# Kernel tuning notes

Measured on AMD Instinct MI355X. Metric: run time of the kernel, lower is better.

## Reference

```python
import jax, jax.numpy as jnp
import numpy as np

NEG = -1e6  # matches torch masked value of -1000000.0
EPS = 1e-5


def setup_inputs() -> dict:
    key = jax.random.key(0)
    k1, k2, k3, k4, k5, k6 = jax.random.split(key, 6)
    B, H, L, D = 2, 16, 2048, 128
    BH = B * H
    return {
        "queries": jax.random.normal(k1, (BH, L, D), dtype=jnp.float32),
        "keys": jax.random.normal(k2, (BH, L, D), dtype=jnp.float32),
        "values": jax.random.normal(k3, (BH, L, D), dtype=jnp.float32),
        "q_mult": jax.random.normal(k4, (B, L, D), dtype=jnp.float32),
        "kv_mult": jax.random.normal(k5, (B, L, D), dtype=jnp.float32),
        "valid_lens": jax.random.randint(k6, (BH,), 0, L, dtype=jnp.int64),
        "num_heads": 16,
    }


def reference(queries, keys, values, q_mult, kv_mult, valid_lens, num_heads):
    # queries/keys/values: [BH, L, d]; q_mult/kv_mult: [B, L, d_m]; valid_lens: [BH]
    d = queries.shape[-1]
    Lk = keys.shape[1]
    scale = 1.0 / jnp.sqrt(jnp.asarray(d, dtype=queries.dtype))
    scores = jnp.einsum('bqd,bkd->bqk', queries, keys) * scale  # [BH, Lq, Lk]

    # custom additive multiplicative-interaction term, Frobenius-normalized per batch element
    mult_ = jnp.einsum('bqd,bkd->bqk', q_mult, kv_mult)  # [B, Lq, Lk]
    fro = jnp.sqrt(jnp.sum(mult_ * mult_, axis=(1, 2), keepdims=True))
    mult_ = mult_ / (fro + EPS)
    mult_ = jnp.repeat(mult_, num_heads, axis=0)  # [BH, Lq, Lk]

    # masked softmax over keys: valid_lens is per-(batch*head), broadcast over queries
    key_mask = jnp.arange(Lk)[None, None, :] < valid_lens[:, None, None]  # [BH, 1, Lk]
    scores = jnp.where(key_mask, scores, NEG)
    attn = jax.nn.softmax(scores, axis=-1) + mult_  # after_softmax=True path

    # dropout is identity (p=0 / eval)
    return jnp.einsum('bqk,bkd->bqd', attn, values)
```

## Files before the change

kernel.cpp:

```cpp
#include <hip/hip_runtime.h>


typedef __attribute__((ext_vector_type(8))) __bf16 bf16x8;
typedef __attribute__((ext_vector_type(16))) float f32x16;
typedef __attribute__((ext_vector_type(4))) unsigned int u32x4;

#define DEV static __device__ __forceinline__

constexpr int LL = 2048, DD = 128, BH = 32;
constexpr float SCALE = 0.08838834764831845f;
constexpr float NEGV = -1e6f;

DEV unsigned pkb(float a, float b) {
  union { __bf16 h[2]; unsigned u; } x;
  x.h[0] = (__bf16)a; x.h[1] = (__bf16)b;
  return x.u;
}
DEV f32x16 mfma32(bf16x8 a, bf16x8 b, f32x16 c) {
  return __builtin_amdgcn_mfma_f32_32x32x16_bf16(a, b, c, 0, 0, 0);
}
DEV void gl16(const void* g, void* l) {
  __builtin_amdgcn_global_load_lds(
      (const __attribute__((address_space(1))) unsigned int*)g,
      (__attribute__((address_space(3))) unsigned int*)l, 16, 0, 0);
}

__global__ __launch_bounds__(256)
void mega_pre(const float* __restrict__ K, const float* __restrict__ V,
              const float* __restrict__ qm, const float* __restrict__ km,
              char* __restrict__ Kb, char* __restrict__ Vt,
              float* __restrict__ Gq, float* __restrict__ Gk,
              float* __restrict__ Mp) {
  __shared__ __align__(16) char smem[16384];
  const int bx = blockIdx.x, tid = threadIdx.x;

  if (bx < 512) {
    float (*skv)[64] = (float(*)[64])smem;
    float (*sv)[128] = (float(*)[128])(smem + 4096);
    int bh = bx & 31, b = bh >> 4, kc = (bx >> 5) & 7, z = (bx >> 8) & 1;
    int l0 = kc * 256;
    int j0 = (tid & 31) * 4, i0 = (tid >> 5) * 8;
    float acc[8][4];
#pragma unroll
    for (int i = 0; i < 8; ++i)
#pragma unroll
      for (int qq = 0; qq < 4; ++qq) acc[i][qq] = 0.f;
    for (int c = 0; c < 16; ++c) {
      __syncthreads();
      {
        int rr = tid >> 4, c4 = (tid & 15) * 4;
        *(float4*)&skv[rr][c4] =
            *(const float4*)(km + (size_t)(b * LL + l0 + c * 16 + rr) * DD + z * 64 + c4);
#pragma unroll
        for (int x = 0; x < 2; ++x) {
          int id2 = x * 256 + tid;
          int r2 = id2 >> 5, c42 = (id2 & 31) * 4;
          *(float4*)&sv[r2][c42] =
              *(const float4*)(V + (size_t)(bh * LL + l0 + c * 16 + r2) * DD + c42);
        }
      }
      __syncthreads();
#pragma unroll
      for (int ll = 0; ll < 16; ++ll) {
        float4 a = *(const float4*)&sv[ll][j0];
        float4 k0 = *(const float4*)&skv[ll][i0];
        float4 k1 = *(const float4*)&skv[ll][i0 + 4];
        float kk[8] = {k0.x, k0.y, k0.z, k0.w, k1.x, k1.y, k1.z, k1.w};
#pragma unroll
        for (int ii = 0; ii < 8; ++ii) {
          acc[ii][0] += kk[ii] * a.x;
          acc[ii][1] += kk[ii] * a.y;
          acc[ii][2] += kk[ii] * a.z;
          acc[ii][3] += kk[ii] * a.w;
        }
      }
    }
    float* dst = Mp + (((size_t)bh * 8 + kc) << 14) + (size_t)(z * 64 + i0) * 128 + j0;
#pragma unroll
    for (int ii = 0; ii < 8; ++ii)
      *(float4*)(dst + (size_t)ii * 128) = *(float4*)&acc[ii][0];

  } else if (bx < 640) {
    float (*s)[128] = (float(*)[128])smem;
    int g = bx - 512;
    int ib = g & 7, lc = (g >> 3) & 3, wb = g >> 5;
    int which = wb >> 1, b = wb & 1;
    const float* A = (which ? km : qm) + (size_t)b * LL * DD;
    float* G = (which ? Gk : Gq) + (size_t)b * DD * DD;
    int i0 = ib * 16 + (tid >> 7) * 8, j = tid & 127;
    int l0 = lc * 512;
    float acc[8];
#pragma unroll
    for (int i = 0; i < 8; ++i) acc[i] = 0.f;
    for (int ch = 0; ch < 16; ++ch) {
      __syncthreads();
#pragma unroll
      for (int i = 0; i < 4; ++i) {
        int c = i * 256 + tid;
        int row = c >> 5, c4 = (c & 31) * 4;
        *(float4*)&s[row][c4] =
            *(const float4*)(A + (size_t)(l0 + ch * 32 + row) * DD + c4);
      }
      __syncthreads();
#pragma unroll
      for (int ll = 0; ll < 32; ++ll) {
        float aj = s[ll][j];
#pragma unroll
        for (int ii = 0; ii < 8; ++ii) acc[ii] += s[ll][i0 + ii] * aj;
      }
    }
#pragma unroll
    for (int ii = 0; ii < 8; ++ii)
      atomicAdd(&G[(size_t)(i0 + ii) * DD + j], acc[ii]);

  } else if (bx < 1664) {
    int pk = bx - 640;
#pragma unroll
    for (int i = 0; i < 4; ++i) {
      int cid = i * 262144 + pk * 256 + tid;
      int h = cid >> 15, k = (cid >> 4) & 2047, c = cid & 15;
      const float* p = K + ((size_t)h * LL + k) * DD + c * 8;
      float4 x0 = *(const float4*)p, x1 = *(const float4*)(p + 4);
      u32x4 v;
      v.x = pkb(x0.x, x0.y); v.y = pkb(x0.z, x0.w);
      v.z = pkb(x1.x, x1.y); v.w = pkb(x1.z, x1.w);
      char* dst = Kb + (((size_t)h * 64 + (k >> 5)) << 13) + ((k & 31) << 8) +
                  ((c ^ (k & 15)) << 4);
      *(u32x4*)dst = v;
    }

  } else {
    float (*sV)[128] = (float(*)[128])smem;
    int pv = bx - 1664;
    int h = pv >> 6, kt = pv & 63;
    const float* src = V + ((size_t)h * LL + kt * 32) * DD;
#pragma unroll
    for (int i = 0; i < 4; ++i) {
      int c = i * 256 + tid;
      int row = c >> 5, c4 = (c & 31) * 4;
      *(float4*)&sV[row][c4] = *(const float4*)(src + (size_t)row * DD + c4);
    }
    __syncthreads();
    char* dstb = Vt + (((size_t)h * 64 + kt) << 13);
#pragma unroll
    for (int i = 0; i < 2; ++i) {
      int c = i * 256 + tid;
      int d = c >> 2, kk8 = c & 3;
      u32x4 v;
      v.x = pkb(sV[kk8 * 8 + 0][d], sV[kk8 * 8 + 1][d]);
      v.y = pkb(sV[kk8 * 8 + 2][d], sV[kk8 * 8 + 3][d]);
      v.z = pkb(sV[kk8 * 8 + 4][d], sV[kk8 * 8 + 5][d]);
      v.w = pkb(sV[kk8 * 8 + 6][d], sV[kk8 * 8 + 7][d]);
      *(u32x4*)(dstb + d * 64 + ((kk8 ^ ((d >> 1) & 3)) << 4)) = v;
    }
  }
}

__global__ __launch_bounds__(256)
void k_post(const float* __restrict__ Gq, const float* __restrict__ Gk,
            float* __restrict__ fro, const float* __restrict__ Mp,
            char* __restrict__ MT) {
  int bx = blockIdx.x, tid = threadIdx.x;
  if (bx < 2) {
    int b = bx;
    const float* gq = Gq + (size_t)b * DD * DD;
    const float* gk = Gk + (size_t)b * DD * DD;
    float acc = 0.f;
    for (int i = tid; i < DD * DD; i += 256) acc += gq[i] * gk[i];
#pragma unroll
    for (int m = 32; m; m >>= 1) acc += __shfl_xor(acc, m);
    __shared__ float sbuf[4];
    if ((tid & 63) == 0) sbuf[tid >> 6] = acc;
    __syncthreads();
    if (tid == 0) fro[b] = sqrtf(sbuf[0] + sbuf[1] + sbuf[2] + sbuf[3]);
  } else {
    int g = bx - 2;
    int bh = g >> 2, kq = (g & 3) * 32;
    int k = kq + (tid >> 3), d0 = (tid & 7) * 16;
    float acc[16];
#pragma unroll
    for (int i = 0; i < 16; ++i) acc[i] = 0.f;
#pragma unroll
    for (int s = 0; s < 8; ++s) {
      const float* p = Mp + (((size_t)bh * 8 + s) << 14) + (size_t)k * 128 + d0;
#pragma unroll
      for (int i = 0; i < 4; ++i) {
        float4 v = *(const float4*)(p + i * 4);
        acc[4 * i + 0] += v.x; acc[4 * i + 1] += v.y;
        acc[4 * i + 2] += v.z; acc[4 * i + 3] += v.w;
      }
    }
    char* dst = MT + (size_t)bh * 32768;
#pragma unroll
    for (int j = 0; j < 16; ++j) {
      int d = d0 + j;
      union { __bf16 h; unsigned short u; } cv;
      cv.h = (__bf16)acc[j];
      *(unsigned short*)(dst + d * 256 + (((k >> 3) ^ (d & 15)) << 4) + (k & 7) * 2) = cv.u;
    }
  }
}

template <int MODE>
__global__ __launch_bounds__(128, 2)
void k_flash(const char* __restrict__ KbG, const char* __restrict__ VtG,
             const char* __restrict__ MT, const float* __restrict__ fro,
             const float* __restrict__ Qf, const float* __restrict__ Kf,
             const float* __restrict__ Vf, const float* __restrict__ qmf,
             const int* __restrict__ vl, float* __restrict__ out) {
  __shared__ __align__(16) char lds[MODE ? 16384 : 32768];

  const int qt = blockIdx.x, bh = blockIdx.y, b = bh >> 4;
  const int tid = threadIdx.x, w = tid >> 6, lane = tid & 63;
  const int r32 = lane & 31, hi = lane >> 5;
  const int vlen = vl[bh];
  const size_t base = (size_t)bh * LL * DD;
  const int q = qt * 64 + w * 32 + r32;

  bf16x8 qfr[8];
#pragma unroll
  for (int ks = 0; ks < 8; ++ks) {
    const float* p = Qf + base + (size_t)q * DD + ks * 16 + hi * 8;
    float4 x0 = *(const float4*)p, x1 = *(const float4*)(p + 4);
    union { unsigned u[4]; bf16x8 v; } u;
    u.u[0] = pkb(x0.x * SCALE, x0.y * SCALE);
    u.u[1] = pkb(x0.z * SCALE, x0.w * SCALE);
    u.u[2] = pkb(x1.x * SCALE, x1.y * SCALE);
    u.u[3] = pkb(x1.z * SCALE, x1.w * SCALE);
    qfr[ks] = u.v;
  }

  f32x16 o[4];
#pragma unroll
  for (int dt = 0; dt < 4; ++dt)
#pragma unroll
    for (int e = 0; e < 16; ++e) o[dt][e] = 0.f;
  float mrun = -3e38f, lrun = 0.f;

  int nt = (vlen == 0) ? 64 : ((vlen + 31) >> 5);

  auto compute = [&](const char* Kl, const char* Vl, int kbase) {
    f32x16 s0;
#pragma unroll
    for (int e = 0; e < 16; ++e) s0[e] = 0.f;
    __builtin_amdgcn_s_setprio(1);
#pragma unroll
    for (int ks = 0; ks < 8; ++ks) {
      bf16x8 a0 = *(const bf16x8*)(Kl + r32 * 256 + (((2 * ks + hi) ^ (r32 & 15)) << 4));
      s0 = mfma32(a0, qfr[ks], s0);
    }
    __builtin_amdgcn_s_setprio(0);

    if (kbase + 32 > vlen) {
#pragma unroll
      for (int e = 0; e < 16; ++e) {
        int k0 = kbase + (e & 3) + 8 * (e >> 2) + 4 * hi;
        if (k0 >= vlen) s0[e] = NEGV;
      }
    }
    f32x16 mx = s0;
#pragma unroll
    for (int st = 8; st; st >>= 1)
#pragma unroll
      for (int e = 0; e < st; ++e) mx[e] = fmaxf(mx[e], mx[e + st]);
    float pm = fmaxf(mx[0], __shfl_xor(mx[0], 32));

    if (!__all(pm <= mrun + 8.f)) {
      float mn = fmaxf(mrun, pm);
      float al = __expf(mrun - mn);
      lrun *= al;
#pragma unroll
      for (int dt = 0; dt < 4; ++dt)
#pragma unroll
        for (int e = 0; e < 16; ++e) o[dt][e] *= al;
      mrun = mn;
    }
#pragma unroll
    for (int e = 0; e < 16; ++e) s0[e] = __expf(s0[e] - mrun);
    f32x16 sm = s0;
#pragma unroll
    for (int st = 8; st; st >>= 1)
#pragma unroll
      for (int e = 0; e < st; ++e) sm[e] += sm[e + st];
    lrun += sm[0];

    bf16x8 PA[2];
#pragma unroll
    for (int ks = 0; ks < 2; ++ks) {
      int bb = ks * 8;
      unsigned x1 = pkb(s0[bb + 0], s0[bb + 1]);
      unsigned x2 = pkb(s0[bb + 2], s0[bb + 3]);
      unsigned y1 = pkb(s0[bb + 4], s0[bb + 5]);
      unsigned y2 = pkb(s0[bb + 6], s0[bb + 7]);
      unsigned sx1 = __shfl_xor(x1, 32), sx2 = __shfl_xor(x2, 32);
      unsigned sy1 = __shfl_xor(y1, 32), sy2 = __shfl_xor(y2, 32);
      union { unsigned u[4]; bf16x8 v; } pu;
      pu.u[0] = hi ? sy1 : x1;
      pu.u[1] = hi ? sy2 : x2;
      pu.u[2] = hi ? y1 : sx1;
      pu.u[3] = hi ? y2 : sx2;
      PA[ks] = pu.v;
    }
    __builtin_amdgcn_s_setprio(1);
#pragma unroll
    for (int dt = 0; dt < 4; ++dt)
#pragma unroll
      for (int ks = 0; ks < 2; ++ks) {
        bf16x8 av = *(const bf16x8*)(Vl + (dt * 32 + r32) * 64 +
                                     (((2 * ks + hi) ^ ((r32 >> 1) & 3)) << 4));
        o[dt] = mfma32(av, PA[ks], o[dt]);
      }
    __builtin_amdgcn_s_setprio(0);
  };

  if (MODE == 0) {
    auto stage = [&](int t, int c2) {
      const char* gk = KbG + (((size_t)bh * 64 + t) << 13) + tid * 16;
      const char* gv = VtG + (((size_t)bh * 64 + t) << 13) + tid * 16;
      char* lk = lds + c2 * 16384 + tid * 16;
      char* lv = lds + c2 * 16384 + 8192 + tid * 16;
#pragma unroll
      for (int i = 0; i < 4; ++i) {
        gl16(gk + i * 2048, lk + i * 2048);
        gl16(gv + i * 2048, lv + i * 2048);
      }
    };
    stage(0, 0);
    __syncthreads();
    int cur = 0;
    for (int t = 0; t < nt; ++t) {
      if (t + 1 < nt) stage(t + 1, cur ^ 1);
      compute(lds + cur * 16384, lds + cur * 16384 + 8192, t * 32);
      __syncthreads();
      cur ^= 1;
    }
  } else {
    char* Kl = lds;
    char* Vl = lds + 8192;
    for (int t = 0; t < nt; ++t) {
      int kbase = t * 32;
#pragma unroll
      for (int i = 0; i < 4; ++i) {
        int c = i * 128 + tid;
        int kk = c >> 4, sl = c & 15;
        const float* p = Kf + base + (size_t)(kbase + kk) * DD + sl * 8;
        float4 x0 = *(const float4*)p, x1 = *(const float4*)(p + 4);
        u32x4 v;
        v.x = pkb(x0.x, x0.y); v.y = pkb(x0.z, x0.w);
        v.z = pkb(x1.x, x1.y); v.w = pkb(x1.z, x1.w);
        *(u32x4*)(Kl + (kk << 8) + ((sl ^ (kk & 15)) << 4)) = v;
      }
#pragma unroll
      for (int i = 0; i < 4; ++i) {
        int c = i * 128 + tid;
        int d = c >> 2, kk8 = c & 3;
        float t0[8];
#pragma unroll
        for (int j = 0; j < 8; ++j)
          t0[j] = Vf[base + (size_t)(kbase + kk8 * 8 + j) * DD + d];
        u32x4 v;
        v.x = pkb(t0[0], t0[1]); v.y = pkb(t0[2], t0[3]);
        v.z = pkb(t0[4], t0[5]); v.w = pkb(t0[6], t0[7]);
        *(u32x4*)(Vl + d * 64 + ((kk8 ^ ((d >> 1) & 3)) << 4)) = v;
      }
      __syncthreads();
      compute(Kl, Vl, kbase);
      __syncthreads();
    }
  }

  float lt = lrun + __shfl_xor(lrun, 32);
  float inv = 1.f / lt;
#pragma unroll
  for (int dt = 0; dt < 4; ++dt)
#pragma unroll
    for (int e = 0; e < 16; ++e) o[dt][e] *= inv;

  if (MODE == 0) {
    float invf = 1.f / (fro[b] + 1e-5f);
    bf16x8 qb[8];
#pragma unroll
    for (int ks = 0; ks < 8; ++ks) {
      const float* p = qmf + ((size_t)b * LL + q) * DD + ks * 16 + hi * 8;
      float4 x0 = *(const float4*)p, x1 = *(const float4*)(p + 4);
      union { unsigned u[4]; bf16x8 v; } u;
      u.u[0] = pkb(x0.x * invf, x0.y * invf);
      u.u[1] = pkb(x0.z * invf, x0.w * invf);
      u.u[2] = pkb(x1.x * invf, x1.y * invf);
      u.u[3] = pkb(x1.z * invf, x1.w * invf);
      qb[ks] = u.v;
    }
    const char* MTb = MT + (size_t)bh * 32768;
#pragma unroll
    for (int kc = 0; kc < 8; ++kc)
#pragma unroll
      for (int dt = 0; dt < 4; ++dt) {
        bf16x8 av = *(const bf16x8*)(MTb + (dt * 32 + r32) * 256 +
                                     (((2 * kc + hi) ^ (r32 & 15)) << 4));
        o[dt] = mfma32(av, qb[kc], o[dt]);
      }
  }

  float* op = out + base + (size_t)q * DD;
#pragma unroll
  for (int dt = 0; dt < 4; ++dt)
#pragma unroll
    for (int rq = 0; rq < 4; ++rq) {
      float4 v;
      v.x = o[dt][4 * rq + 0];
      v.y = o[dt][4 * rq + 1];
      v.z = o[dt][4 * rq + 2];
      v.w = o[dt][4 * rq + 3];
      *(float4*)(op + dt * 32 + rq * 8 + hi * 4) = v;
    }
}

__global__ void k_gram(const float* __restrict__ qm, const float* __restrict__ km,
                       float* __restrict__ Gq, float* __restrict__ Gk) {
  int which = blockIdx.z >> 1, b = blockIdx.z & 1;
  const float* A = (which ? km : qm) + (size_t)b * LL * DD;
  float* G = (which ? Gk : Gq) + (size_t)b * DD * DD;
  int i0 = blockIdx.x * 8;
  int l0 = blockIdx.y * 512;
  __shared__ float s[32][128];
  float acc[8];
#pragma unroll
  for (int i = 0; i < 8; ++i) acc[i] = 0.f;
  for (int ch = 0; ch < 16; ++ch) {
    __syncthreads();
    for (int rr = 0; rr < 32; ++rr)
      s[rr][threadIdx.x] = A[(size_t)(l0 + ch * 32 + rr) * DD + threadIdx.x];
    __syncthreads();
    for (int ll = 0; ll < 32; ++ll) {
      float aj = s[ll][threadIdx.x];
#pragma unroll
      for (int ii = 0; ii < 8; ++ii) acc[ii] += s[ll][i0 + ii] * aj;
    }
  }
#pragma unroll
  for (int ii = 0; ii < 8; ++ii)
    atomicAdd(&G[(size_t)(i0 + ii) * DD + threadIdx.x], acc[ii]);
}

__global__ void k_fro(const float* __restrict__ Gq, const float* __restrict__ Gk,
                      float* __restrict__ fro) {
  int b = blockIdx.x;
  const float* gq = Gq + (size_t)b * DD * DD;
  const float* gk = Gk + (size_t)b * DD * DD;
  float acc = 0.f;
  for (int i = threadIdx.x; i < DD * DD; i += 256) acc += gq[i] * gk[i];
#pragma unroll
  for (int m = 32; m; m >>= 1) acc += __shfl_xor(acc, m);
  __shared__ float sbuf[4];
  if ((threadIdx.x & 63) == 0) sbuf[threadIdx.x >> 6] = acc;
  __syncthreads();
  if (threadIdx.x == 0) fro[b] = sqrtf(sbuf[0] + sbuf[1] + sbuf[2] + sbuf[3]);
}

__global__ void k_M_atomic(const float* __restrict__ km, const float* __restrict__ Vf,
                           float* __restrict__ M) {
  int bh = blockIdx.x, b = bh >> 4;
  int l0 = blockIdx.y * 128;
  __shared__ float skv[16][128];
  __shared__ float sv[16][128];
  int j0 = (threadIdx.x & 31) * 4;
  int i0 = (threadIdx.x >> 5) * 16;
  float acc[16][4];
#pragma unroll
  for (int i = 0; i < 16; ++i)
#pragma unroll
    for (int qq = 0; qq < 4; ++qq) acc[i][qq] = 0.f;
  for (int c = 0; c < 8; ++c) {
    __syncthreads();
    for (int x = 0; x < 8; ++x) {
      int idx = x * 256 + threadIdx.x;
      int rr = idx >> 7, cc = idx & 127;
      skv[rr][cc] = km[(size_t)(b * LL + l0 + c * 16 + rr) * DD + cc];
      sv[rr][cc] = Vf[(size_t)(bh * LL + l0 + c * 16 + rr) * DD + cc];
    }
    __syncthreads();
    for (int ll = 0; ll < 16; ++ll) {
      float a0 = sv[ll][j0], a1 = sv[ll][j0 + 1];
      float a2 = sv[ll][j0 + 2], a3 = sv[ll][j0 + 3];
#pragma unroll
      for (int ii = 0; ii < 16; ++ii) {
        float kv = skv[ll][i0 + ii];
        acc[ii][0] += kv * a0;
        acc[ii][1] += kv * a1;
        acc[ii][2] += kv * a2;
        acc[ii][3] += kv * a3;
      }
    }
  }
#pragma unroll
  for (int ii = 0; ii < 16; ++ii)
#pragma unroll
    for (int qq = 0; qq < 4; ++qq)
      atomicAdd(&M[(size_t)bh * DD * DD + (size_t)(i0 + ii) * DD + j0 + qq],
                acc[ii][qq]);
}

__global__ void k_multadd(const float* __restrict__ qm, const float* __restrict__ M,
                          const float* __restrict__ fro, float* __restrict__ out) {
  int bh = blockIdx.y, b = bh >> 4;
  int l = blockIdx.x * 128 + (threadIdx.x & 127);
  int dh = (threadIdx.x >> 7) * 64;
  float inv = 1.0f / (fro[b] + 1e-5f);
  const float* qrow = qm + ((size_t)b * LL + l) * DD;
  const float* Mb = M + (size_t)bh * DD * DD + dh;
  float acc[64];
#pragma unroll
  for (int i = 0; i < 64; ++i) acc[i] = 0.f;
  for (int k = 0; k < 128; ++k) {
    float qv = qrow[k];
    const float4* m4 = (const float4*)(Mb + (size_t)k * DD);
#pragma unroll
    for (int i = 0; i < 16; ++i) {
      float4 mm = m4[i];
      acc[4 * i + 0] += qv * mm.x;
      acc[4 * i + 1] += qv * mm.y;
      acc[4 * i + 2] += qv * mm.z;
      acc[4 * i + 3] += qv * mm.w;
    }
  }
  float* op = out + ((size_t)bh * LL + l) * DD + dh;
#pragma unroll
  for (int i = 0; i < 16; ++i) {
    float4 ov = ((float4*)op)[i];
    ov.x += acc[4 * i + 0] * inv;
    ov.y += acc[4 * i + 1] * inv;
    ov.z += acc[4 * i + 2] * inv;
    ov.w += acc[4 * i + 3] * inv;
    ((float4*)op)[i] = ov;
  }
}

extern "C" void kernel_launch(void* const* d_in, const int* in_sizes, int n_in,
                              void* d_out, int out_size, void* d_ws, size_t ws_size,
                              hipStream_t stream) {
  (void)in_sizes; (void)n_in; (void)out_size;
  const float* Q = (const float*)d_in[0];
  const float* K = (const float*)d_in[1];
  const float* V = (const float*)d_in[2];
  const float* qm = (const float*)d_in[3];
  const float* km = (const float*)d_in[4];
  const int* vl = (const int*)d_in[5];
  float* out = (float*)d_out;

  char* ws = (char*)d_ws;
  const size_t off_Gq = 0;
  const size_t off_Gk = 131072;
  const size_t off_fro = 262144;
  const size_t off_MT = 294912;
  const size_t off_Kb = off_MT + 1048576;
  const size_t szb = (size_t)BH * LL * DD * 2;
  const size_t off_Vt = off_Kb + szb;
  const size_t off_end = off_Vt + szb;
  bool fits = ws_size >= off_end;

  float* Gq = (float*)(ws + off_Gq);
  float* Gk = (float*)(ws + off_Gk);
  float* fro = (float*)(ws + off_fro);
  char* MT = ws + off_MT;

  if (fits) {
    float* Mp = (float*)d_out;
    hipMemsetAsync(ws, 0, off_fro + 256, stream);
    mega_pre<<<3712, 256, 0, stream>>>(K, V, qm, km, ws + off_Kb, ws + off_Vt,
                                       Gq, Gk, Mp);
    k_post<<<130, 256, 0, stream>>>(Gq, Gk, fro, Mp, MT);
    k_flash<0><<<dim3(32, 32), 128, 0, stream>>>(ws + off_Kb, ws + off_Vt, MT, fro,
                                                 Q, K, V, qm, vl, out);
  } else {
    float* Mw = (float*)(ws + off_MT);
    hipMemsetAsync(ws, 0, off_MT + 2097152, stream);
    k_gram<<<dim3(16, 4, 4), 128, 0, stream>>>(qm, km, Gq, Gk);
    k_fro<<<2, 256, 0, stream>>>(Gq, Gk, fro);
    k_flash<1><<<dim3(32, 32), 128, 0, stream>>>(nullptr, nullptr, nullptr, nullptr,
                                                 Q, K, V, qm, vl, out);
    k_M_atomic<<<dim3(32, 16), 256, 0, stream>>>(km, V, Mw);
    k_multadd<<<dim3(16, 32), 256, 0, stream>>>(qm, Mw, fro, out);
  }
}
```

Before: 173.1 us.

## Use single-wave flash blocks and replace block barriers with vmcnt waits

The flash kernel now runs one 64-lane wavefront per block, each covering 32 queries, on a grid with twice as many blocks. Because a block has a single wave, the __syncthreads barriers around the K/V staging are removed. Explicit s_waitcnt vmcnt waits on the async global-to-LDS loads take their place, so the next tile's prefetch can overlap compute. The cost is that each block loads the full K/V tiles for only 32 queries, doubling LDS fill traffic per query. LDS per block is unchanged, which may limit occupancy.

```diff
diff --git a/kernel.cpp b/kernel.cpp
--- a/kernel.cpp
+++ b/kernel.cpp
@@ -202,7 +202,7 @@
 }
 
 template <int MODE>
-__global__ __launch_bounds__(128, 2)
+__global__ __launch_bounds__(64)
 void k_flash(const char* __restrict__ KbG, const char* __restrict__ VtG,
              const char* __restrict__ MT, const float* __restrict__ fro,
              const float* __restrict__ Qf, const float* __restrict__ Kf,
@@ -211,11 +211,11 @@
   __shared__ __align__(16) char lds[MODE ? 16384 : 32768];
 
   const int qt = blockIdx.x, bh = blockIdx.y, b = bh >> 4;
-  const int tid = threadIdx.x, w = tid >> 6, lane = tid & 63;
+  const int lane = threadIdx.x;
   const int r32 = lane & 31, hi = lane >> 5;
   const int vlen = vl[bh];
   const size_t base = (size_t)bh * LL * DD;
-  const int q = qt * 64 + w * 32 + r32;
+  const int q = qt * 32 + r32;
 
   bf16x8 qfr[8];
 #pragma unroll
@@ -315,23 +315,27 @@
 
   if (MODE == 0) {
     auto stage = [&](int t, int c2) {
-      const char* gk = KbG + (((size_t)bh * 64 + t) << 13) + tid * 16;
-      const char* gv = VtG + (((size_t)bh * 64 + t) << 13) + tid * 16;
-      char* lk = lds + c2 * 16384 + tid * 16;
-      char* lv = lds + c2 * 16384 + 8192 + tid * 16;
-#pragma unroll
-      for (int i = 0; i < 4; ++i) {
-        gl16(gk + i * 2048, lk + i * 2048);
-        gl16(gv + i * 2048, lv + i * 2048);
+      const char* gk = KbG + (((size_t)bh * 64 + t) << 13) + lane * 16;
+      const char* gv = VtG + (((size_t)bh * 64 + t) << 13) + lane * 16;
+      char* lk = lds + c2 * 16384 + lane * 16;
+      char* lv = lds + c2 * 16384 + 8192 + lane * 16;
+#pragma unroll
+      for (int i = 0; i < 8; ++i) {
+        gl16(gk + i * 1024, lk + i * 1024);
+        gl16(gv + i * 1024, lv + i * 1024);
       }
     };
     stage(0, 0);
-    __syncthreads();
     int cur = 0;
     for (int t = 0; t < nt; ++t) {
-      if (t + 1 < nt) stage(t + 1, cur ^ 1);
+      if (t + 1 < nt) {
+        stage(t + 1, cur ^ 1);
+        asm volatile("s_waitcnt vmcnt(16)" ::: "memory");
+      } else {
+        asm volatile("s_waitcnt vmcnt(0)" ::: "memory");
+      }
+      __builtin_amdgcn_sched_barrier(0);
       compute(lds + cur * 16384, lds + cur * 16384 + 8192, t * 32);
-      __syncthreads();
       cur ^= 1;
     }
   } else {
@@ -340,32 +344,30 @@
     for (int t = 0; t < nt; ++t) {
       int kbase = t * 32;
 #pragma unroll
-      for (int i = 0; i < 4; ++i) {
-        int c = i * 128 + tid;
-        int kk = c >> 4, sl = c & 15;
-        const float* p = Kf + base + (size_t)(kbase + kk) * DD + sl * 8;
+      for (int i = 0; i < 8; ++i) {
+        int idx = i * 64 + lane;
+        int kk = idx >> 4, c = idx & 15;
+        const float* p = Kf + base + (size_t)(kbase + kk) * DD + c * 8;
         float4 x0 = *(const float4*)p, x1 = *(const float4*)(p + 4);
         u32x4 v;
         v.x = pkb(x0.x, x0.y); v.y = pkb(x0.z, x0.w);
         v.z = pkb(x1.x, x1.y); v.w = pkb(x1.z, x1.w);
-        *(u32x4*)(Kl + (kk << 8) + ((sl ^ (kk & 15)) << 4)) = v;
-      }
-#pragma unroll
-      for (int i = 0; i < 4; ++i) {
-        int c = i * 128 + tid;
-        int d = c >> 2, kk8 = c & 3;
+        *(u32x4*)(Kl + (kk << 8) + ((c ^ (kk & 15)) << 4)) = v;
+      }
+#pragma unroll
+      for (int i = 0; i < 8; ++i) {
+        int cid = i * 64 + lane;
+        int d = cid & 127, kg = cid >> 7;
         float t0[8];
 #pragma unroll
         for (int j = 0; j < 8; ++j)
-          t0[j] = Vf[base + (size_t)(kbase + kk8 * 8 + j) * DD + d];
+          t0[j] = Vf[base + (size_t)(kbase + kg * 8 + j) * DD + d];
         u32x4 v;
         v.x = pkb(t0[0], t0[1]); v.y = pkb(t0[2], t0[3]);
         v.z = pkb(t0[4], t0[5]); v.w = pkb(t0[6], t0[7]);
-        *(u32x4*)(Vl + d * 64 + ((kk8 ^ ((d >> 1) & 3)) << 4)) = v;
-      }
-      __syncthreads();
+        *(u32x4*)(Vl + d * 64 + ((kg ^ ((d >> 1) & 3)) << 4)) = v;
+      }
       compute(Kl, Vl, kbase);
-      __syncthreads();
     }
   }
 
@@ -569,15 +571,15 @@
     mega_pre<<<3712, 256, 0, stream>>>(K, V, qm, km, ws + off_Kb, ws + off_Vt,
                                        Gq, Gk, Mp);
     k_post<<<130, 256, 0, stream>>>(Gq, Gk, fro, Mp, MT);
-    k_flash<0><<<dim3(32, 32), 128, 0, stream>>>(ws + off_Kb, ws + off_Vt, MT, fro,
-                                                 Q, K, V, qm, vl, out);
+    k_flash<0><<<dim3(64, 32), 64, 0, stream>>>(ws + off_Kb, ws + off_Vt, MT, fro,
+                                                Q, K, V, qm, vl, out);
   } else {
     float* Mw = (float*)(ws + off_MT);
     hipMemsetAsync(ws, 0, off_MT + 2097152, stream);
     k_gram<<<dim3(16, 4, 4), 128, 0, stream>>>(qm, km, Gq, Gk);
     k_fro<<<2, 256, 0, stream>>>(Gq, Gk, fro);
-    k_flash<1><<<dim3(32, 32), 128, 0, stream>>>(nullptr, nullptr, nullptr, nullptr,
-                                                 Q, K, V, qm, vl, out);
+    k_flash<1><<<dim3(64, 32), 64, 0, stream>>>(nullptr, nullptr, nullptr, nullptr,
+                                                Q, K, V, qm, vl, out);
     k_M_atomic<<<dim3(32, 16), 256, 0, stream>>>(km, V, Mw);
     k_multadd<<<dim3(16, 32), 256, 0, stream>>>(qm, Mw, fro, out);
   }
```

Measured after the change: 205.0 us. 1.18x slower.
